# Kernel tuning notes

Hardware: AMD Instinct MI355X
Metric: run time of the kernel (lower is better)

Reference implementation:

```python
import jax, jax.numpy as jnp
import numpy as np

N_NODES = 100000
N_EDGES = 1600000
NFEAT = 64
NHID = 64
NCLASS = 16


def setup_inputs() -> dict:
    key = jax.random.key(0)
    k_x, k_e, k_w1, k_b1, k_w2, k_b2 = jax.random.split(key, 6)
    x = jax.random.normal(k_x, (N_NODES, NFEAT), dtype=jnp.float32)
    edge_index = jax.random.randint(k_e, (2, N_EDGES), 0, N_NODES, dtype=jnp.int64)
    # Glorot-ish init for the GIN update MLP
    W1 = jax.random.normal(k_w1, (NFEAT, NHID), dtype=jnp.float32) * (1.0 / np.sqrt(NFEAT))
    b1 = jnp.zeros((NHID,), dtype=jnp.float32)
    W2 = jax.random.normal(k_w2, (NHID, NCLASS), dtype=jnp.float32) * (1.0 / np.sqrt(NHID))
    b2 = jnp.zeros((NCLASS,), dtype=jnp.float32)
    eps = jnp.float32(0.0)  # train_eps=True, initialized to 0
    return {"x": x, "edge_index": edge_index, "eps": eps,
            "W1": W1, "b1": b1, "W2": W2, "b2": b2}


def reference(x, edge_index, eps, W1, b1, W2, b2):
    # GINConv: out = MLP((1 + eps) * x + sum_{j in N(i)} x_j)
    src = edge_index[0]  # message source nodes
    dst = edge_index[1]  # aggregation targets (source_to_target flow)
    agg = jax.ops.segment_sum(x[src], dst, num_segments=x.shape[0])  # [N, F]
    h = (1.0 + eps) * x + agg
    # MLP([nfeat, nhid, nclass]): Linear -> ReLU -> (dropout=identity in eval) -> Linear
    h = jax.nn.relu(h @ W1 + b1)
    return h @ W2 + b2
```

## Files before the change

### kernel.cpp

```cpp
#include <hip/hip_runtime.h>
#include <hip/hip_bf16.h>
#include <hip/hip_fp16.h>


#define NFEAT 64
#define NHID 64
#define NCLASS 16

#define PCAP 6144
#define MAXBUCK 512
#define PT 512
#define PEPT 8
#define ST 1024
#define SEPT 6

__global__ __launch_bounds__(512) void k_cvt(
    const float4* __restrict__ x4, uint2* __restrict__ xh,
    int* __restrict__ cursor, int n4, int nbuck)
{
    int i = blockIdx.x * 512 + threadIdx.x;
    if (i < n4) {
        float4 v = x4[i];
        __half2 a = __floats2half2_rn(v.x, v.y);
        __half2 b = __floats2half2_rn(v.z, v.w);
        uint2 o;
        o.x = *reinterpret_cast<unsigned int*>(&a);
        o.y = *reinterpret_cast<unsigned int*>(&b);
        xh[i] = o;
    }
    if (blockIdx.x == 0 && threadIdx.x < nbuck)
        cursor[threadIdx.x] = threadIdx.x * PCAP;
}

__global__ __launch_bounds__(PT) void k_part(
    const int* __restrict__ ei, int* __restrict__ cursor,
    int* __restrict__ dsts, int n_edges, int nbuck)
{
    __shared__ int lcnt[MAXBUCK];
    __shared__ int sbase[MAXBUCK];
    int tid = threadIdx.x;
    for (int i = tid; i < nbuck; i += PT) lcnt[i] = 0;
    __syncthreads();

    int e0 = blockIdx.x * (PT * PEPT);
    int bk[PEPT], rk[PEPT], pk[PEPT];
    #pragma unroll
    for (int k = 0; k < PEPT; ++k) {
        int e = e0 + k * PT + tid;
        if (e < n_edges) {
            int src = ei[e];
            int dst = ei[n_edges + e];
            int b = dst >> 8;
            bk[k] = b;
            pk[k] = (src << 8) | (dst & 255);
            rk[k] = atomicAdd(&lcnt[b], 1);
        } else bk[k] = -1;
    }
    __syncthreads();
    for (int i = tid; i < nbuck; i += PT)
        sbase[i] = lcnt[i] ? atomicAdd(&cursor[i], lcnt[i]) : 0;
    __syncthreads();
    #pragma unroll
    for (int k = 0; k < PEPT; ++k)
        if (bk[k] >= 0) dsts[sbase[bk[k]] + rk[k]] = pk[k];
}

__global__ __launch_bounds__(ST) void k_bsort(
    const int* __restrict__ dsts, const int* __restrict__ cursor,
    int* __restrict__ csr_src,
    int* __restrict__ row_start, int* __restrict__ row_end, int n_nodes)
{
    __shared__ int cnt[256];
    __shared__ int off[256];
    int b = blockIdx.x;
    int tid = threadIdx.x, lane = tid & 63, wid = tid >> 6;
    int s = cursor[b] - b * PCAP;
    int gin = b * PCAP;
    if (tid < 256) cnt[tid] = 0;
    __syncthreads();

    int dk[SEPT], rk[SEPT], sk[SEPT];
    #pragma unroll
    for (int k = 0; k < SEPT; ++k) {
        int i = k * ST + tid;
        if (i < s) {
            int p = dsts[gin + i];
            int d = p & 255;
            dk[k] = d;
            sk[k] = p >> 8;
            rk[k] = atomicAdd(&cnt[d], 1);
        } else dk[k] = -1;
    }
    __syncthreads();
    if (wid == 0) {
        int c0 = cnt[lane * 4], c1 = cnt[lane * 4 + 1], c2 = cnt[lane * 4 + 2], c3 = cnt[lane * 4 + 3];
        int p1 = c0, p2 = p1 + c1, p3 = p2 + c2, p4 = p3 + c3;
        int ss = p4;
        #pragma unroll
        for (int o = 1; o < 64; o <<= 1) {
            int u = __shfl_up(ss, o);
            if (lane >= o) ss += u;
        }
        int base = ss - p4;
        off[lane * 4] = base; off[lane * 4 + 1] = base + p1;
        off[lane * 4 + 2] = base + p2; off[lane * 4 + 3] = base + p3;
    }
    __syncthreads();
    int bb = b * PCAP;
    #pragma unroll
    for (int k = 0; k < SEPT; ++k)
        if (dk[k] >= 0) csr_src[bb + off[dk[k]] + rk[k]] = sk[k];
    int node = b * 256 + tid;
    if (tid < 256 && node < n_nodes) {
        row_start[node] = bb + off[tid];
        row_end[node]   = bb + off[tid] + cnt[tid];
    }
}

__global__ __launch_bounds__(512) void k_gather_mlp(
    const float4* __restrict__ x4,
    const uint2* __restrict__ xh,
    const int* __restrict__ row_start,
    const int* __restrict__ row_end,
    const int* __restrict__ csr_src,
    const float* __restrict__ eps_p,
    const float* __restrict__ W1,
    const float* __restrict__ b1,
    const float* __restrict__ W2,
    const float* __restrict__ b2,
    float* __restrict__ out,
    int n_nodes)
{
    __shared__ float sW1[NFEAT * NHID];
    __shared__ float sW2[NHID * 17];
    __shared__ float sb1[NHID];
    __shared__ float sb2[NCLASS];
    __shared__ float sh0[32][68];
    __shared__ float sh1[32][68];
    __shared__ int   sIdx[8][64];

    int tid = threadIdx.x;
    for (int i = tid; i < NFEAT * NHID; i += 512) sW1[i] = W1[i];
    for (int i = tid; i < NHID * NCLASS; i += 512) sW2[(i >> 4) * 17 + (i & 15)] = W2[i];
    if (tid < NHID) sb1[tid] = b1[tid];
    if (tid < NCLASS) sb2[tid] = b2[tid];
    __syncthreads();

    float eps1 = 1.0f + eps_p[0];
    int wave = tid >> 6;
    int lane = tid & 63;
    int q = lane >> 4;
    int f = lane & 15;
    int s8 = (lane >> 3) & 1;
    int f8 = lane & 7;
    int nloc = wave * 4 + q;

    for (int nb0 = blockIdx.x * 32; nb0 < n_nodes; nb0 += gridDim.x * 32) {
        int myNode = nb0 + nloc;
        bool valid = myNode < n_nodes;
        int s = 0, e = 0;
        if (valid) { s = row_start[myNode]; e = row_end[myNode]; }
        int dmax = e - s;
        dmax = max(dmax, __shfl_xor(dmax, 16));
        dmax = max(dmax, __shfl_xor(dmax, 32));

        float4 accA = make_float4(0.f, 0.f, 0.f, 0.f);
        float4 accB = make_float4(0.f, 0.f, 0.f, 0.f);
        for (int base = 0; base < dmax; base += 16) {
            int p = s + base + f;
            sIdx[wave][lane] = (p < e) ? csr_src[p] : -1;
            #pragma unroll
            for (int t = 0; t < 8; ++t) {
                int idx = sIdx[wave][q * 16 + t * 2 + s8];
                if (idx >= 0) {
                    const uint4* rp = (const uint4*)(xh + (size_t)idx * 16);
                    uint4 u = rp[f8];
                    __half2 h0 = *reinterpret_cast<__half2*>(&u.x);
                    __half2 h1 = *reinterpret_cast<__half2*>(&u.y);
                    __half2 h2 = *reinterpret_cast<__half2*>(&u.z);
                    __half2 h3 = *reinterpret_cast<__half2*>(&u.w);
                    float2 g0 = __half22float2(h0);
                    float2 g1 = __half22float2(h1);
                    float2 g2 = __half22float2(h2);
                    float2 g3 = __half22float2(h3);
                    accA.x += g0.x; accA.y += g0.y; accA.z += g1.x; accA.w += g1.y;
                    accB.x += g2.x; accB.y += g2.y; accB.z += g3.x; accB.w += g3.y;
                }
            }
        }
        accA.x += __shfl_xor(accA.x, 8); accA.y += __shfl_xor(accA.y, 8);
        accA.z += __shfl_xor(accA.z, 8); accA.w += __shfl_xor(accA.w, 8);
        accB.x += __shfl_xor(accB.x, 8); accB.y += __shfl_xor(accB.y, 8);
        accB.z += __shfl_xor(accB.z, 8); accB.w += __shfl_xor(accB.w, 8);
        if (s8 == 0) {
            if (valid) {
                float4 xa = x4[(size_t)myNode * 16 + f8 * 2];
                float4 xb = x4[(size_t)myNode * 16 + f8 * 2 + 1];
                accA.x += eps1 * xa.x; accA.y += eps1 * xa.y;
                accA.z += eps1 * xa.z; accA.w += eps1 * xa.w;
                accB.x += eps1 * xb.x; accB.y += eps1 * xb.y;
                accB.z += eps1 * xb.z; accB.w += eps1 * xb.w;
            }
            *(float4*)&sh0[nloc][f8 * 8] = accA;
            *(float4*)&sh0[nloc][f8 * 8 + 4] = accB;
        }

        int r = wave * 4;
        float a0 = sb1[lane], a1 = a0, a2 = a0, a3 = a0;
        #pragma unroll
        for (int kk = 0; kk < 16; ++kk) {
            float4 h0 = *(const float4*)&sh0[r + 0][kk * 4];
            float4 h1v = *(const float4*)&sh0[r + 1][kk * 4];
            float4 h2 = *(const float4*)&sh0[r + 2][kk * 4];
            float4 h3 = *(const float4*)&sh0[r + 3][kk * 4];
            #pragma unroll
            for (int i = 0; i < 4; ++i) {
                float w = sW1[(kk * 4 + i) * NHID + lane];
                a0 += ((const float*)&h0)[i] * w;
                a1 += ((const float*)&h1v)[i] * w;
                a2 += ((const float*)&h2)[i] * w;
                a3 += ((const float*)&h3)[i] * w;
            }
        }
        sh1[r + 0][lane] = fmaxf(a0, 0.f);
        sh1[r + 1][lane] = fmaxf(a1, 0.f);
        sh1[r + 2][lane] = fmaxf(a2, 0.f);
        sh1[r + 3][lane] = fmaxf(a3, 0.f);

        float o = sb2[f];
        #pragma unroll
        for (int jj = 0; jj < 16; ++jj) {
            float4 hv = *(const float4*)&sh1[nloc][jj * 4];
            o += hv.x * sW2[(jj * 4 + 0) * 17 + f];
            o += hv.y * sW2[(jj * 4 + 1) * 17 + f];
            o += hv.z * sW2[(jj * 4 + 2) * 17 + f];
            o += hv.w * sW2[(jj * 4 + 3) * 17 + f];
        }
        if (valid) out[(size_t)myNode * NCLASS + f] = o;
    }
}

extern "C" void kernel_launch(void* const* d_in, const int* in_sizes, int n_in,
                              void* d_out, int out_size, void* d_ws, size_t ws_size,
                              hipStream_t stream) {
    const float* x   = (const float*)d_in[0];
    const int*   ei  = (const int*)d_in[1];
    const float* eps = (const float*)d_in[2];
    const float* W1  = (const float*)d_in[3];
    const float* b1  = (const float*)d_in[4];
    const float* W2  = (const float*)d_in[5];
    const float* b2  = (const float*)d_in[6];
    float* out = (float*)d_out;

    int n_nodes = in_sizes[0] / NFEAT;
    int n_edges = in_sizes[1] / 2;
    int nbuck = (n_nodes + 255) / 256;

    char* ws = (char*)d_ws;
    int* cursor    = (int*)ws;
    int* dsts      = (int*)(ws + 4096);
    size_t o_rs    = 4096 + (size_t)nbuck * PCAP * 4;
    int* row_start = (int*)(ws + o_rs);
    int* row_end   = (int*)(ws + o_rs + 400128);
    int* csr_src   = (int*)(ws + o_rs + 800256);
    size_t o_xh    = o_rs + 800256 + (size_t)nbuck * PCAP * 4;
    o_xh = (o_xh + 15) & ~(size_t)15;
    uint2* xh      = (uint2*)(ws + o_xh);

    int n4 = n_nodes * 16;
    k_cvt<<<(n4 + 511) / 512, 512, 0, stream>>>((const float4*)x, xh, cursor, n4, nbuck);
    k_part<<<(n_edges + PT * PEPT - 1) / (PT * PEPT), PT, 0, stream>>>(
        ei, cursor, dsts, n_edges, nbuck);
    k_bsort<<<nbuck, ST, 0, stream>>>(dsts, cursor, csr_src, row_start, row_end, n_nodes);
    int ntile = (n_nodes + 31) / 32;
    int ngrid = ntile < 1024 ? ntile : 1024;
    k_gather_mlp<<<ngrid, 512, 0, stream>>>(
        (const float4*)x, xh, row_start, row_end, csr_src, eps, W1, b1, W2, b2, out, n_nodes);
}
```

Baseline: 183.6 us.

## Stage partition and bucket-sort scatters in LDS for coalesced global writes

The partition kernel now computes a block-local prefix sum over bucket counts, places each edge into LDS in bucket order, and then writes them out contiguously per bucket, so the global scatter is coalesced instead of random. The bucket-sort kernel likewise builds the sorted source list in LDS and copies it to global memory linearly. The cost is more LDS use (about 24KB extra per partition block), extra barriers and a serial 8-way scan. The partition kernel also assumes nbuck is at most 512, since it hardcodes 512 buckets and reads lcnt for every thread.

```diff
diff --git a/kernel.cpp b/kernel.cpp
--- a/kernel.cpp
+++ b/kernel.cpp
@@ -8,7 +8,6 @@
 #define NCLASS 16
 
 #define PCAP 6144
-#define MAXBUCK 512
 #define PT 512
 #define PEPT 8
 #define ST 1024
@@ -36,10 +35,15 @@
     const int* __restrict__ ei, int* __restrict__ cursor,
     int* __restrict__ dsts, int n_edges, int nbuck)
 {
-    __shared__ int lcnt[MAXBUCK];
-    __shared__ int sbase[MAXBUCK];
+    __shared__ int lcnt[512];
+    __shared__ int loff[512];
+    __shared__ int sbase[512];
+    __shared__ int sw[8];
+    __shared__ int val[PT * PEPT];
+    __shared__ unsigned short bid[PT * PEPT];
     int tid = threadIdx.x;
-    for (int i = tid; i < nbuck; i += PT) lcnt[i] = 0;
+    int lane = tid & 63, wid = tid >> 6;
+    lcnt[tid] = 0;
     __syncthreads();
 
     int e0 = blockIdx.x * (PT * PEPT);
@@ -57,12 +61,33 @@
         } else bk[k] = -1;
     }
     __syncthreads();
-    for (int i = tid; i < nbuck; i += PT)
-        sbase[i] = lcnt[i] ? atomicAdd(&cursor[i], lcnt[i]) : 0;
+    int v = lcnt[tid];
+    int s = v;
+    #pragma unroll
+    for (int off = 1; off < 64; off <<= 1) {
+        int u = __shfl_up(s, off);
+        if (lane >= off) s += u;
+    }
+    if (lane == 63) sw[wid] = s;
+    sbase[tid] = v ? atomicAdd(&cursor[tid], v) : 0;
+    __syncthreads();
+    if (tid == 0) { int a = 0; for (int i = 0; i < 8; ++i) { int t2 = sw[i]; sw[i] = a; a += t2; } }
+    __syncthreads();
+    loff[tid] = (s - v) + sw[wid];
     __syncthreads();
     #pragma unroll
     for (int k = 0; k < PEPT; ++k)
-        if (bk[k] >= 0) dsts[sbase[bk[k]] + rk[k]] = pk[k];
+        if (bk[k] >= 0) {
+            int p = loff[bk[k]] + rk[k];
+            val[p] = pk[k];
+            bid[p] = (unsigned short)bk[k];
+        }
+    __syncthreads();
+    int ntot = loff[511] + lcnt[511];
+    for (int i = tid; i < ntot; i += PT) {
+        int b = bid[i];
+        dsts[sbase[b] + (i - loff[b])] = val[i];
+    }
 }
 
 __global__ __launch_bounds__(ST) void k_bsort(
@@ -72,6 +97,7 @@
 {
     __shared__ int cnt[256];
     __shared__ int off[256];
+    __shared__ int lval[PCAP];
     int b = blockIdx.x;
     int tid = threadIdx.x, lane = tid & 63, wid = tid >> 6;
     int s = cursor[b] - b * PCAP;
@@ -106,10 +132,12 @@
         off[lane * 4 + 2] = base + p2; off[lane * 4 + 3] = base + p3;
     }
     __syncthreads();
+    #pragma unroll
+    for (int k = 0; k < SEPT; ++k)
+        if (dk[k] >= 0) lval[off[dk[k]] + rk[k]] = sk[k];
+    __syncthreads();
     int bb = b * PCAP;
-    #pragma unroll
-    for (int k = 0; k < SEPT; ++k)
-        if (dk[k] >= 0) csr_src[bb + off[dk[k]] + rk[k]] = sk[k];
+    for (int i = tid; i < s; i += ST) csr_src[bb + i] = lval[i];
     int node = b * 256 + tid;
     if (tid < 256 && node < n_nodes) {
         row_start[node] = bb + off[tid];
```

Result: faster. 173.8 us (median of 2 runs) (-5.3%).
